# Performance work log

Measured on AMD Instinct MI355X. Metric: run time of the kernel, lower is better.

Reference implementation:

```python
import jax, jax.numpy as jnp
import numpy as np

N_PP = 100000   # papers
N_A = 50000     # authors
N_AP = N_PP + N_A
DIM = 16
B = 8192        # sampled node set sizes
E = 500000      # edges per modality
ALPHA = 0.5
EPS = 1e-12


def _cdist(x, y):
    # Euclidean cdist via quadratic expansion (avoids [N,M,d] intermediate)
    sq = (jnp.sum(x * x, -1)[:, None] + jnp.sum(y * y, -1)[None, :]
          - 2.0 * x @ y.T)
    return jnp.sqrt(jnp.maximum(sq, EPS))


def _pdist(x, y):
    d = x - y
    return jnp.sqrt(jnp.sum(d * d, -1) + EPS)


def setup_inputs() -> dict:
    key = jax.random.key(0)
    ks = jax.random.split(key, 10)
    u = lambda k, s: jax.random.uniform(k, s, jnp.float32, -1.0, 1.0)  # 2*rand-1
    p = u(ks[0], (N_PP, DIM))
    p_star = u(ks[1], (N_PP, DIM))
    a = u(ks[2], (N_A, DIM))
    beta_ap = u(ks[3], (N_AP,))
    gamma_pp = u(ks[4], (2 * N_PP,))
    edges_pp = jax.random.randint(ks[5], (2, E), 0, N_PP, jnp.int32)
    e_ap0 = jax.random.randint(ks[6], (1, E), 0, N_PP, jnp.int32)
    e_ap1 = jax.random.randint(ks[7], (1, E), N_PP, N_AP, jnp.int32)
    edges_ap = jnp.concatenate([e_ap0, e_ap1], 0)
    p_star_nodes = jnp.sort(jax.random.randint(ks[8], (B,), 0, N_PP, jnp.int32))
    kk = jax.random.split(ks[9], 2)
    p_nodes = jax.random.randint(kk[0], (B,), 0, N_PP, jnp.int32)
    a_nodes = jax.random.randint(kk[1], (B,), N_PP, N_AP, jnp.int32)
    return {"p": p, "p_star": p_star, "a": a, "beta_ap": beta_ap,
            "gamma_pp": gamma_pp, "edges_pp": edges_pp, "edges_ap": edges_ap,
            "p_star_nodes": p_star_nodes, "p_nodes": p_nodes, "a_nodes": a_nodes}


def reference(p, p_star, a, beta_ap, gamma_pp,
              edges_pp, edges_ap, p_star_nodes, p_nodes, a_nodes):
    # ---- pp modality ----
    # link term over edges (edges[0]=p_star idx, edges[1]=p idx)
    link_pp = jnp.sum(gamma_pp[edges_pp[0]] + gamma_pp[edges_pp[1] + N_PP]
                      - _pdist(p_star[edges_pp[0]], p[edges_pp[1]]))
    # non-link term: [B_pstar, B_p] matrix, upper-triangular (k=1) masked sum
    g_ps = gamma_pp[p_star_nodes]                 # [B]
    g_p = gamma_pp[p_nodes + N_PP]                # [B]
    mat_pp = g_ps[:, None] + g_p[None, :]         # == gamma_mat.T in torch code
    dist_pp = _cdist(p_star[p_star_nodes], p[p_nodes])
    nonlink_pp = jnp.sum(jnp.triu(jnp.exp(mat_pp - dist_pp), k=1))
    nll_pp = -(link_pp - nonlink_pp)

    # ---- ap modality ----
    link_ap = jnp.sum(beta_ap[edges_ap[0]] + beta_ap[edges_ap[1]]
                      - _pdist(p_star[edges_ap[0]], a[edges_ap[1] - N_PP]))
    b_ps = beta_ap[p_star_nodes]
    b_a = beta_ap[a_nodes]
    mat_ap = b_ps[:, None] + b_a[None, :]         # == beta_mat.T
    dist_ap = _cdist(p_star[p_star_nodes], a[a_nodes - N_PP])
    nonlink_ap = jnp.sum(jnp.exp(mat_ap - dist_ap))
    nll_ap = -(link_ap - nonlink_ap)

    # average batch loss as in __train_one_batch
    loss = ALPHA * nll_pp / B + (1.0 - ALPHA) * nll_ap / B
    return loss
```

## Files before the change

kernel.cpp:

```cpp
#include <hip/hip_runtime.h>

#define N_PP 100000
#define N_A  50000
#define NEDGE 500000
#define BSZ 8192
#define TILE 128
#define SCALE 1.44269504088896f
#define QS 127.0f
#define QSI (1.0f / 127.0f)

#define GRID_P 2048
#define EB 977
#define PP_JOBS 2080
#define AP_JOBS 4096
#define PJOBS (PP_JOBS + AP_JOBS)

#define GRID_FB 2048

typedef __attribute__((ext_vector_type(8)))  short bf16x8;
typedef __attribute__((ext_vector_type(16))) float f32x16;
typedef __attribute__((ext_vector_type(4)))  float f32x4;
typedef unsigned short u16;

#if __has_builtin(__builtin_amdgcn_sqrtf)
#define FAST_SQRT(x) __builtin_amdgcn_sqrtf(x)
#else
#define FAST_SQRT(x) sqrtf(x)
#endif
#if __has_builtin(__builtin_amdgcn_exp2f)
#define FAST_EXP2(x) __builtin_amdgcn_exp2f(x)
#else
#define FAST_EXP2(x) exp2f(x)
#endif

__device__ __forceinline__ u16 f2bf(float f) {
    unsigned u = __builtin_bit_cast(unsigned, f);
    u += 0x7FFFu + ((u >> 16) & 1u);
    return (u16)(u >> 16);
}
__device__ __forceinline__ float bf2f(u16 s) {
    unsigned u = ((unsigned)s) << 16;
    return __builtin_bit_cast(float, u);
}

__device__ __forceinline__ bf16x8 load_frag_f32(const float* __restrict__ src) {
    float4 v0 = *(const float4*)src;
    float4 v1 = *(const float4*)(src + 4);
    bf16x8 f;
    f[0] = (short)f2bf(v0.x); f[1] = (short)f2bf(v0.y);
    f[2] = (short)f2bf(v0.z); f[3] = (short)f2bf(v0.w);
    f[4] = (short)f2bf(v1.x); f[5] = (short)f2bf(v1.y);
    f[6] = (short)f2bf(v1.z); f[7] = (short)f2bf(v1.w);
    return f;
}

__device__ __forceinline__ int dot4i8(int a, int b, int c) {
#if __has_builtin(__builtin_amdgcn_sdot4)
    return __builtin_amdgcn_sdot4(a, b, c, false);
#else
    int s = c;
#pragma unroll
    for (int k = 0; k < 4; ++k) {
        int av = (int)(signed char)(a >> (8 * k));
        int bv = (int)(signed char)(b >> (8 * k));
        s += av * bv;
    }
    return s;
#endif
}

__device__ __forceinline__ float dist_i8(const int* __restrict__ ra,
                                         const int* __restrict__ rb) {
    int4 qa = *(const int4*)ra;
    int4 qb = *(const int4*)rb;
    int dot = dot4i8(qa.x, qb.x, 0);
    dot = dot4i8(qa.y, qb.y, dot);
    dot = dot4i8(qa.z, qb.z, dot);
    dot = dot4i8(qa.w, qb.w, dot);
    int na = dot4i8(qa.x, qa.x, 0);
    na = dot4i8(qa.y, qa.y, na);
    na = dot4i8(qa.z, qa.z, na);
    na = dot4i8(qa.w, qa.w, na);
    int nb = dot4i8(qb.x, qb.x, 0);
    nb = dot4i8(qb.y, qb.y, nb);
    nb = dot4i8(qb.z, qb.z, nb);
    nb = dot4i8(qb.w, qb.w, nb);
    int d2 = na + nb - 2 * dot;
    return FAST_SQRT((float)d2) * QSI;
}

__device__ __forceinline__ float pdist16_f32(const float* __restrict__ xv,
                                             const float* __restrict__ yv) {
    float d2 = 1e-12f;
#pragma unroll
    for (int c = 0; c < 16; c += 4) {
        float4 xq = *(const float4*)(xv + c);
        float4 yq = *(const float4*)(yv + c);
        float dx = xq.x - yq.x; d2 = fmaf(dx, dx, d2);
        float dy = xq.y - yq.y; d2 = fmaf(dy, dy, d2);
        float dz = xq.z - yq.z; d2 = fmaf(dz, dz, d2);
        float dw = xq.w - yq.w; d2 = fmaf(dw, dw, d2);
    }
    return sqrtf(d2);
}

__device__ __forceinline__ unsigned packq4(float a, float b, float c, float d) {
    int qa = (int)rintf(a * QS), qb = (int)rintf(b * QS);
    int qc = (int)rintf(c * QS), qd = (int)rintf(d * QS);
    return (unsigned)(qa & 0xFF) | ((unsigned)(qb & 0xFF) << 8)
         | ((unsigned)(qc & 0xFF) << 16) | ((unsigned)(qd & 0xFF) << 24);
}

__global__ __launch_bounds__(256) void prep_kernel(
        const float* __restrict__ p, const float* __restrict__ p_star,
        const float* __restrict__ a, const float* __restrict__ beta,
        const float* __restrict__ gamma,
        const int* __restrict__ psn, const int* __restrict__ pn,
        const int* __restrict__ an,
        int* __restrict__ ps8, int* __restrict__ p8, int* __restrict__ a8,
        u16* __restrict__ Xb, u16* __restrict__ Yp, u16* __restrict__ Ya,
        float* __restrict__ Xxx, float* __restrict__ Xg,
        float* __restrict__ Pyy, float* __restrict__ Pg,
        float* __restrict__ Ayy, float* __restrict__ Ag)
{
    const int NITEMS = 250000 + 3 * BSZ;
    for (int i = blockIdx.x * 256 + threadIdx.x; i < NITEMS; i += gridDim.x * 256) {
        if (i < 250000) {
            const float* src; int* dst;
            if (i < 100000)      { src = p_star + (size_t)i * 16;       dst = ps8 + (size_t)i * 4; }
            else if (i < 200000) { src = p + (size_t)(i - 100000) * 16; dst = p8 + (size_t)(i - 100000) * 4; }
            else                 { src = a + (size_t)(i - 200000) * 16; dst = a8 + (size_t)(i - 200000) * 4; }
            float4 v0 = *(const float4*)src;
            float4 v1 = *(const float4*)(src + 4);
            float4 v2 = *(const float4*)(src + 8);
            float4 v3 = *(const float4*)(src + 12);
            int4 q;
            q.x = (int)packq4(v0.x, v0.y, v0.z, v0.w);
            q.y = (int)packq4(v1.x, v1.y, v1.z, v1.w);
            q.z = (int)packq4(v2.x, v2.y, v2.z, v2.w);
            q.w = (int)packq4(v3.x, v3.y, v3.z, v3.w);
            *(int4*)dst = q;
        } else {
            const int j = i - 250000;
            const int which = j >> 13;
            const int r = j & (BSZ - 1);
            const float* src; float wsc; u16* drow; float* xxp; float* gp;
            if (which == 0) {
                int node = psn[r]; src = p_star + (size_t)node * 16;
                wsc = gamma[node] * SCALE; drow = Xb + (size_t)r * 16; xxp = Xxx; gp = Xg;
            } else if (which == 1) {
                int node = pn[r]; src = p + (size_t)node * 16;
                wsc = gamma[node + N_PP] * SCALE; drow = Yp + (size_t)r * 16; xxp = Pyy; gp = Pg;
            } else {
                int node = an[r]; src = a + (size_t)(node - N_PP) * 16;
                wsc = beta[node] * SCALE; drow = Ya + (size_t)r * 16; xxp = Ayy; gp = Ag;
            }
            bf16x8 lo = load_frag_f32(src);
            bf16x8 hi = load_frag_f32(src + 8);
            *(bf16x8*)drow = lo;
            *(bf16x8*)(drow + 8) = hi;
            float ss = 0.f;
#pragma unroll
            for (int c = 0; c < 8; ++c) {
                float q0 = bf2f((u16)lo[c]); ss = fmaf(q0, q0, ss);
                float q1 = bf2f((u16)hi[c]); ss = fmaf(q1, q1, ss);
            }
            xxp[r] = ss;
            gp[r] = wsc;
        }
    }
}

__global__ __launch_bounds__(256) void edge_kernel(
        const float* __restrict__ gamma, const float* __restrict__ beta,
        const int* __restrict__ edges_pp, const int* __restrict__ edges_ap,
        const int* __restrict__ ps8, const int* __restrict__ p8,
        const int* __restrict__ a8, float* __restrict__ epart)
{
    const int t = threadIdx.x;
    const int base = blockIdx.x * 512;
    float sppl = 0.f, sapl = 0.f;
#pragma unroll
    for (int k = 0; k < 2; ++k) {
        int i = base + k * 256 + t;
        if (i < NEDGE) {
            int e0 = __builtin_nontemporal_load(edges_pp + i);
            int e1 = __builtin_nontemporal_load(edges_pp + NEDGE + i);
            int f0 = __builtin_nontemporal_load(edges_ap + i);
            int f1 = __builtin_nontemporal_load(edges_ap + NEDGE + i);
            sppl += gamma[e0] + gamma[e1 + N_PP]
                  - dist_i8(ps8 + (size_t)e0 * 4, p8 + (size_t)e1 * 4);
            sapl += beta[f0] + beta[f1]
                  - dist_i8(ps8 + (size_t)f0 * 4, a8 + (size_t)(f1 - N_PP) * 4);
        }
    }
    __shared__ float red[4][2];
    const int l = t & 63, w = t >> 6;
#pragma unroll
    for (int o = 32; o > 0; o >>= 1) {
        sppl += __shfl_down(sppl, o, 64);
        sapl += __shfl_down(sapl, o, 64);
    }
    if (l == 0) { red[w][0] = sppl; red[w][1] = sapl; }
    __syncthreads();
    if (t < 2)
        epart[(size_t)blockIdx.x * 2 + t] =
            red[0][t] + red[1][t] + red[2][t] + red[3][t];
}

template <bool DIAG>
__device__ __forceinline__ float epi_rt(
        const f32x16& ca, const f32x16& cb,
        const float* __restrict__ xxg, const float* __restrict__ gxg,
        int rb, float yy0, float gy0, float yy1, float gy1,
        int cj0, int cj1)
{
    f32x4 xxq[4], gxq[4];
#pragma unroll
    for (int q = 0; q < 4; ++q) {
        xxq[q] = *(const f32x4*)&xxg[rb + q * 8];
        gxq[q] = *(const f32x4*)&gxg[rb + q * 8];
    }
    float s = 0.f;
#pragma unroll
    for (int q = 0; q < 4; ++q) {
#pragma unroll
        for (int j = 0; j < 4; ++j) {
            const int reg = q * 4 + j;
            float sxy = xxq[q][j];
            float gx  = gxq[q][j];
            float sq0 = fmaf(-2.f, ca[reg], sxy + yy0);
            float d0  = FAST_SQRT(fmaxf(sq0, 1e-12f));
            float v0  = FAST_EXP2(fmaf(-SCALE, d0, gx + gy0));
            float sq1 = fmaf(-2.f, cb[reg], sxy + yy1);
            float d1  = FAST_SQRT(fmaxf(sq1, 1e-12f));
            float v1  = FAST_EXP2(fmaf(-SCALE, d1, gx + gy1));
            if (DIAG) {
                int row = rb + q * 8 + j;
                v0 = (cj0 > row) ? v0 : 0.f;
                v1 = (cj1 > row) ? v1 : 0.f;
            }
            s += v0 + v1;
        }
    }
    return s;
}

__global__ __launch_bounds__(256) void pair_kernel(
        const u16* __restrict__ Xb, const u16* __restrict__ Yp,
        const u16* __restrict__ Ya,
        const float* __restrict__ Xxx, const float* __restrict__ Xg,
        const float* __restrict__ Pyy, const float* __restrict__ Pg,
        const float* __restrict__ Ayy, const float* __restrict__ Ag,
        float* __restrict__ ppart)
{
    const int t = threadIdx.x;
    const int l = t & 63, w = t >> 6;
    const int wr = w >> 1, wc = w & 1;
    const int l31 = l & 31, h = l >> 5;

    float s_ppn = 0.f, s_apn = 0.f;

    for (int j = blockIdx.x; j < PJOBS; j += gridDim.x) {
        const bool pp = (j < PP_JOBS);
        int bx, by;
        if (pp) {
            int k = j;
            float disc = sqrtf((float)(129 * 129 - 8 * k));
            by = (int)((129.0f - disc) * 0.5f);
            while (64 * by - (by * (by - 1)) / 2 > k) --by;
            while (64 * (by + 1) - ((by + 1) * by) / 2 <= k) ++by;
            bx = by + (k - (64 * by - (by * (by - 1)) / 2));
        } else {
            int k = j - PP_JOBS;
            bx = k & 63; by = k >> 6;
        }
        const bool diag = pp && (bx == by);

        const u16* Ytab = pp ? Yp : Ya;
        const float* yyP = (pp ? Pyy : Ayy) + bx * TILE;
        const float* gyP = (pp ? Pg  : Ag ) + bx * TILE;
        const int ar0 = by * TILE + wr * 64 + l31;
        const int bc0 = bx * TILE + wc * 64 + l31;
        bf16x8 aF0 = *(const bf16x8*)(Xb   + (size_t)ar0 * 16 + h * 8);
        bf16x8 aF1 = *(const bf16x8*)(Xb   + (size_t)(ar0 + 32) * 16 + h * 8);
        bf16x8 bF0 = *(const bf16x8*)(Ytab + (size_t)bc0 * 16 + h * 8);
        bf16x8 bF1 = *(const bf16x8*)(Ytab + (size_t)(bc0 + 32) * 16 + h * 8);
        const float* xxg = Xxx + by * TILE;
        const float* gxg = Xg  + by * TILE;
        const int cj0 = wc * 64 + l31, cj1 = cj0 + 32;
        const float yy0 = yyP[cj0], gy0 = gyP[cj0];
        const float yy1 = yyP[cj1], gy1 = gyP[cj1];
        const int rb0 = wr * 64 + 4 * h, rb1 = rb0 + 32;

        f32x16 c00, c01, c10, c11;
#pragma unroll
        for (int i = 0; i < 16; ++i) { c00[i] = 0.f; c01[i] = 0.f; c10[i] = 0.f; c11[i] = 0.f; }
        c00 = __builtin_amdgcn_mfma_f32_32x32x16_bf16(aF0, bF0, c00, 0, 0, 0);
        c01 = __builtin_amdgcn_mfma_f32_32x32x16_bf16(aF0, bF1, c01, 0, 0, 0);
        c10 = __builtin_amdgcn_mfma_f32_32x32x16_bf16(aF1, bF0, c10, 0, 0, 0);
        c11 = __builtin_amdgcn_mfma_f32_32x32x16_bf16(aF1, bF1, c11, 0, 0, 0);

        float sum;
        if (diag) {
            sum = epi_rt<true >(c00, c01, xxg, gxg, rb0, yy0, gy0, yy1, gy1, cj0, cj1)
                + epi_rt<true >(c10, c11, xxg, gxg, rb1, yy0, gy0, yy1, gy1, cj0, cj1);
        } else {
            sum = epi_rt<false>(c00, c01, xxg, gxg, rb0, yy0, gy0, yy1, gy1, cj0, cj1)
                + epi_rt<false>(c10, c11, xxg, gxg, rb1, yy0, gy0, yy1, gy1, cj0, cj1);
        }
        if (pp) s_ppn += sum; else s_apn += sum;
    }

    __shared__ float red[4][2];
#pragma unroll
    for (int o = 32; o > 0; o >>= 1) {
        s_ppn += __shfl_down(s_ppn, o, 64);
        s_apn += __shfl_down(s_apn, o, 64);
    }
    if (l == 0) { red[w][0] = s_ppn; red[w][1] = s_apn; }
    __syncthreads();
    if (t < 2)
        ppart[(size_t)blockIdx.x * 2 + t] =
            red[0][t] + red[1][t] + red[2][t] + red[3][t];
}

__global__ __launch_bounds__(256) void finalize_split(
        const float* __restrict__ epart, const float* __restrict__ ppart,
        float* __restrict__ out)
{
    __shared__ double acc4[4];
    const int t = threadIdx.x;
    const int c = t >> 6, l = t & 63;
    double s = 0.0;
    if (c == 0)      { for (int i = l; i < EB; i += 64)     s += (double)epart[(size_t)i * 2 + 0]; }
    else if (c == 1) { for (int i = l; i < GRID_P; i += 64) s += (double)ppart[(size_t)i * 2 + 0]; }
    else if (c == 2) { for (int i = l; i < EB; i += 64)     s += (double)epart[(size_t)i * 2 + 1]; }
    else             { for (int i = l; i < GRID_P; i += 64) s += (double)ppart[(size_t)i * 2 + 1]; }
#pragma unroll
    for (int o = 32; o > 0; o >>= 1) s += __shfl_down(s, o, 64);
    if (l == 0) acc4[c] = s;
    __syncthreads();
    if (t == 0) {
        double nll_pp = -(acc4[0] - acc4[1]);
        double nll_ap = -(acc4[2] - acc4[3]);
        out[0] = (float)(0.5 * nll_pp / (double)BSZ + 0.5 * nll_ap / (double)BSZ);
    }
}

__global__ __launch_bounds__(256) void fused_fb(
        const float* __restrict__ p, const float* __restrict__ p_star,
        const float* __restrict__ a, const float* __restrict__ beta,
        const float* __restrict__ gamma,
        const int* __restrict__ edges_pp, const int* __restrict__ edges_ap,
        const int* __restrict__ psn, const int* __restrict__ pn,
        const int* __restrict__ an, float* __restrict__ partials)
{
    const int t = threadIdx.x;
    const int l = t & 63, w = t >> 6;
    const int wr = w >> 1, wc = w & 1;
    const int l31 = l & 31, h = l >> 5;

    __shared__ float sxx[TILE], sgx[TILE], syy[TILE], sgy[TILE];
    __shared__ float red4[4][4];

    float s_ppl = 0.f, s_ppn = 0.f, s_apl = 0.f, s_apn = 0.f;
    const int NJ = EB + PP_JOBS + AP_JOBS;

    for (int j = blockIdx.x; j < NJ; j += gridDim.x) {
        if (j < EB) {
            const int base = j * 512;
#pragma unroll
            for (int k = 0; k < 2; ++k) {
                int i = base + k * 256 + t;
                if (i < NEDGE) {
                    int e0 = edges_pp[i], e1 = edges_pp[NEDGE + i];
                    int f0 = edges_ap[i], f1 = edges_ap[NEDGE + i];
                    s_ppl += gamma[e0] + gamma[e1 + N_PP]
                           - pdist16_f32(p_star + (size_t)e0 * 16, p + (size_t)e1 * 16);
                    s_apl += beta[f0] + beta[f1]
                           - pdist16_f32(p_star + (size_t)f0 * 16, a + (size_t)(f1 - N_PP) * 16);
                }
            }
        } else {
            const bool pp = (j < EB + PP_JOBS);
            int bx, by;
            if (pp) {
                int k = j - EB;
                float disc = sqrtf((float)(129 * 129 - 8 * k));
                by = (int)((129.0f - disc) * 0.5f);
                while (64 * by - (by * (by - 1)) / 2 > k) --by;
                while (64 * (by + 1) - ((by + 1) * by) / 2 <= k) ++by;
                bx = by + (k - (64 * by - (by * (by - 1)) / 2));
            } else {
                int k = j - EB - PP_JOBS;
                bx = k & 63; by = k >> 6;
            }
            const bool diag = pp && (bx == by);
            const float* Y  = pp ? p : a;
            const float* wv = pp ? gamma : beta;
            const int* yn   = pp ? pn : an;
            const int wyo   = pp ? N_PP : 0;
            const int yvo   = pp ? 0 : -N_PP;
            const int ar0 = by * TILE + wr * 64 + l31;
            const int an0 = psn[ar0], an1 = psn[ar0 + 32];
            bf16x8 aF0 = load_frag_f32(p_star + (size_t)an0 * 16 + h * 8);
            bf16x8 aF1 = load_frag_f32(p_star + (size_t)an1 * 16 + h * 8);
            const int bc0g = bx * TILE + wc * 64 + l31;
            const int bn0 = yn[bc0g], bn1 = yn[bc0g + 32];
            bf16x8 bF0 = load_frag_f32(Y + (size_t)(bn0 + yvo) * 16 + h * 8);
            bf16x8 bF1 = load_frag_f32(Y + (size_t)(bn1 + yvo) * 16 + h * 8);
            {
                const bool isx = (t < 128);
                const int  r   = isx ? t : t - 128;
                const int  node = isx ? psn[by * TILE + r] : yn[bx * TILE + r];
                const float* src = isx ? (p_star + (size_t)node * 16)
                                       : (Y + (size_t)(node + yvo) * 16);
                float ss = 0.f;
#pragma unroll
                for (int c = 0; c < 16; c += 4) {
                    float4 v = *(const float4*)(src + c);
                    float q0 = bf2f(f2bf(v.x)), q1 = bf2f(f2bf(v.y));
                    float q2 = bf2f(f2bf(v.z)), q3 = bf2f(f2bf(v.w));
                    ss = fmaf(q0, q0, ss); ss = fmaf(q1, q1, ss);
                    ss = fmaf(q2, q2, ss); ss = fmaf(q3, q3, ss);
                }
                if (isx) { sxx[r] = ss; sgx[r] = wv[node] * SCALE; }
                else     { syy[r] = ss; sgy[r] = wv[node + wyo] * SCALE; }
            }
            __syncthreads();
            const int cj0 = wc * 64 + l31, cj1 = cj0 + 32;
            const float yy0 = syy[cj0], gy0 = sgy[cj0];
            const float yy1 = syy[cj1], gy1 = sgy[cj1];
            const int rb0 = wr * 64 + 4 * h, rb1 = rb0 + 32;

            f32x16 c00, c01, c10, c11;
#pragma unroll
            for (int i = 0; i < 16; ++i) { c00[i] = 0.f; c01[i] = 0.f; c10[i] = 0.f; c11[i] = 0.f; }
            c00 = __builtin_amdgcn_mfma_f32_32x32x16_bf16(aF0, bF0, c00, 0, 0, 0);
            c01 = __builtin_amdgcn_mfma_f32_32x32x16_bf16(aF0, bF1, c01, 0, 0, 0);
            c10 = __builtin_amdgcn_mfma_f32_32x32x16_bf16(aF1, bF0, c10, 0, 0, 0);
            c11 = __builtin_amdgcn_mfma_f32_32x32x16_bf16(aF1, bF1, c11, 0, 0, 0);

            float sum;
            if (diag) {
                sum = epi_rt<true >(c00, c01, sxx, sgx, rb0, yy0, gy0, yy1, gy1, cj0, cj1)
                    + epi_rt<true >(c10, c11, sxx, sgx, rb1, yy0, gy0, yy1, gy1, cj0, cj1);
            } else {
                sum = epi_rt<false>(c00, c01, sxx, sgx, rb0, yy0, gy0, yy1, gy1, cj0, cj1)
                    + epi_rt<false>(c10, c11, sxx, sgx, rb1, yy0, gy0, yy1, gy1, cj0, cj1);
            }
            if (pp) s_ppn += sum; else s_apn += sum;
            __syncthreads();
        }
    }

    float v4[4] = {s_ppl, s_ppn, s_apl, s_apn};
#pragma unroll
    for (int c = 0; c < 4; ++c) {
        float r = v4[c];
#pragma unroll
        for (int o = 32; o > 0; o >>= 1) r += __shfl_down(r, o, 64);
        if (l == 0) red4[w][c] = r;
    }
    __syncthreads();
    if (t < 4)
        partials[(size_t)blockIdx.x * 4 + t] =
            red4[0][t] + red4[1][t] + red4[2][t] + red4[3][t];
}

__global__ __launch_bounds__(256) void finalize_fb(
        const float* __restrict__ partials, float* __restrict__ out)
{
    __shared__ double acc4[4];
    const int t = threadIdx.x;
    const int c = t >> 6, l = t & 63;
    double s = 0.0;
    for (int i = l; i < GRID_FB; i += 64) s += (double)partials[(size_t)i * 4 + c];
#pragma unroll
    for (int o = 32; o > 0; o >>= 1) s += __shfl_down(s, o, 64);
    if (l == 0) acc4[c] = s;
    __syncthreads();
    if (t == 0) {
        double nll_pp = -(acc4[0] - acc4[1]);
        double nll_ap = -(acc4[2] - acc4[3]);
        out[0] = (float)(0.5 * nll_pp / (double)BSZ + 0.5 * nll_ap / (double)BSZ);
    }
}

extern "C" void kernel_launch(void* const* d_in, const int* in_sizes, int n_in,
                              void* d_out, int out_size, void* d_ws, size_t ws_size,
                              hipStream_t stream)
{
    const float* p       = (const float*)d_in[0];
    const float* p_star  = (const float*)d_in[1];
    const float* a       = (const float*)d_in[2];
    const float* beta    = (const float*)d_in[3];
    const float* gamma   = (const float*)d_in[4];
    const int* edges_pp  = (const int*)d_in[5];
    const int* edges_ap  = (const int*)d_in[6];
    const int* psn       = (const int*)d_in[7];
    const int* pn        = (const int*)d_in[8];
    const int* an        = (const int*)d_in[9];

    char* ws = (char*)d_ws;
    size_t off = 0;
    float* ppart = (float*)(ws + off); off += (size_t)GRID_P * 2 * sizeof(float);
    float* epart = (float*)(ws + off); off += (size_t)EB * 2 * sizeof(float);
    int* ps8 = (int*)(ws + off); off += (size_t)100000 * 16;
    int* p8  = (int*)(ws + off); off += (size_t)100000 * 16;
    int* a8  = (int*)(ws + off); off += (size_t)50000 * 16;
    u16* Xb  = (u16*)(ws + off); off += (size_t)BSZ * 32;
    u16* Yp  = (u16*)(ws + off); off += (size_t)BSZ * 32;
    u16* Ya  = (u16*)(ws + off); off += (size_t)BSZ * 32;
    float* Xxx = (float*)(ws + off); off += BSZ * 4;
    float* Xg  = (float*)(ws + off); off += BSZ * 4;
    float* Pyy = (float*)(ws + off); off += BSZ * 4;
    float* Pg  = (float*)(ws + off); off += BSZ * 4;
    float* Ayy = (float*)(ws + off); off += BSZ * 4;
    float* Ag  = (float*)(ws + off); off += BSZ * 4;
    const bool packed = (ws_size >= off);

    if (packed) {
        prep_kernel<<<256, 256, 0, stream>>>(
            p, p_star, a, beta, gamma, psn, pn, an,
            ps8, p8, a8, Xb, Yp, Ya, Xxx, Xg, Pyy, Pg, Ayy, Ag);
        edge_kernel<<<EB, 256, 0, stream>>>(
            gamma, beta, edges_pp, edges_ap, ps8, p8, a8, epart);
        pair_kernel<<<GRID_P, 256, 0, stream>>>(
            Xb, Yp, Ya, Xxx, Xg, Pyy, Pg, Ayy, Ag, ppart);
        finalize_split<<<1, 256, 0, stream>>>(epart, ppart, (float*)d_out);
    } else {
        float* fbpart = (float*)ws;
        fused_fb<<<GRID_FB, 256, 0, stream>>>(
            p, p_star, a, beta, gamma, edges_pp, edges_ap, psn, pn, an, fbpart);
        finalize_fb<<<1, 256, 0, stream>>>(fbpart, (float*)d_out);
    }
}
```

Baseline: 86.25 us.

## Merge edge and pair kernels into one interleaved work kernel

Fuses the edge-sum kernel and the MFMA pair kernel into a single launch. Every third block among the first 3*EB handles an edge chunk and the rest run pair jobs, so memory-bound gather work shares the GPU with compute-bound tiles. This is meant to remove one launch and the idle tail between the two kernels. The prep kernel grid is also doubled. Register and LDS usage become the maximum of both paths, which could lower occupancy.

```diff
diff --git a/kernel.cpp b/kernel.cpp
--- a/kernel.cpp
+++ b/kernel.cpp
@@ -9,8 +9,9 @@
 #define QS 127.0f
 #define QSI (1.0f / 127.0f)
 
+#define EB 977
 #define GRID_P 2048
-#define EB 977
+#define GRID_W (3 * EB + GRID_P - EB)
 #define PP_JOBS 2080
 #define AP_JOBS 4096
 #define PJOBS (PP_JOBS + AP_JOBS)
@@ -171,43 +172,6 @@
     }
 }
 
-__global__ __launch_bounds__(256) void edge_kernel(
-        const float* __restrict__ gamma, const float* __restrict__ beta,
-        const int* __restrict__ edges_pp, const int* __restrict__ edges_ap,
-        const int* __restrict__ ps8, const int* __restrict__ p8,
-        const int* __restrict__ a8, float* __restrict__ epart)
-{
-    const int t = threadIdx.x;
-    const int base = blockIdx.x * 512;
-    float sppl = 0.f, sapl = 0.f;
-#pragma unroll
-    for (int k = 0; k < 2; ++k) {
-        int i = base + k * 256 + t;
-        if (i < NEDGE) {
-            int e0 = __builtin_nontemporal_load(edges_pp + i);
-            int e1 = __builtin_nontemporal_load(edges_pp + NEDGE + i);
-            int f0 = __builtin_nontemporal_load(edges_ap + i);
-            int f1 = __builtin_nontemporal_load(edges_ap + NEDGE + i);
-            sppl += gamma[e0] + gamma[e1 + N_PP]
-                  - dist_i8(ps8 + (size_t)e0 * 4, p8 + (size_t)e1 * 4);
-            sapl += beta[f0] + beta[f1]
-                  - dist_i8(ps8 + (size_t)f0 * 4, a8 + (size_t)(f1 - N_PP) * 4);
-        }
-    }
-    __shared__ float red[4][2];
-    const int l = t & 63, w = t >> 6;
-#pragma unroll
-    for (int o = 32; o > 0; o >>= 1) {
-        sppl += __shfl_down(sppl, o, 64);
-        sapl += __shfl_down(sapl, o, 64);
-    }
-    if (l == 0) { red[w][0] = sppl; red[w][1] = sapl; }
-    __syncthreads();
-    if (t < 2)
-        epart[(size_t)blockIdx.x * 2 + t] =
-            red[0][t] + red[1][t] + red[2][t] + red[3][t];
-}
-
 template <bool DIAG>
 __device__ __forceinline__ float epi_rt(
         const f32x16& ca, const f32x16& cb,
@@ -246,22 +210,61 @@
     return s;
 }
 
-__global__ __launch_bounds__(256) void pair_kernel(
+__global__ __launch_bounds__(256) void work_kernel(
+        const float* __restrict__ gamma, const float* __restrict__ beta,
+        const int* __restrict__ edges_pp, const int* __restrict__ edges_ap,
+        const int* __restrict__ ps8, const int* __restrict__ p8,
+        const int* __restrict__ a8,
         const u16* __restrict__ Xb, const u16* __restrict__ Yp,
         const u16* __restrict__ Ya,
         const float* __restrict__ Xxx, const float* __restrict__ Xg,
         const float* __restrict__ Pyy, const float* __restrict__ Pg,
         const float* __restrict__ Ayy, const float* __restrict__ Ag,
-        float* __restrict__ ppart)
-{
+        float* __restrict__ epart, float* __restrict__ ppart)
+{
+    const int b = blockIdx.x;
     const int t = threadIdx.x;
     const int l = t & 63, w = t >> 6;
+
+    if ((b % 3 == 0) && (b / 3 < EB)) {
+        const int base = (b / 3) * 512;
+        float sppl = 0.f, sapl = 0.f;
+#pragma unroll
+        for (int k = 0; k < 2; ++k) {
+            int i = base + k * 256 + t;
+            if (i < NEDGE) {
+                int e0 = __builtin_nontemporal_load(edges_pp + i);
+                int e1 = __builtin_nontemporal_load(edges_pp + NEDGE + i);
+                int f0 = __builtin_nontemporal_load(edges_ap + i);
+                int f1 = __builtin_nontemporal_load(edges_ap + NEDGE + i);
+                sppl += gamma[e0] + gamma[e1 + N_PP]
+                      - dist_i8(ps8 + (size_t)e0 * 4, p8 + (size_t)e1 * 4);
+                sapl += beta[f0] + beta[f1]
+                      - dist_i8(ps8 + (size_t)f0 * 4, a8 + (size_t)(f1 - N_PP) * 4);
+            }
+        }
+        __shared__ float rede[4][2];
+#pragma unroll
+        for (int o = 32; o > 0; o >>= 1) {
+            sppl += __shfl_down(sppl, o, 64);
+            sapl += __shfl_down(sapl, o, 64);
+        }
+        if (l == 0) { rede[w][0] = sppl; rede[w][1] = sapl; }
+        __syncthreads();
+        if (t < 2)
+            epart[(size_t)(b / 3) * 2 + t] =
+                rede[0][t] + rede[1][t] + rede[2][t] + rede[3][t];
+        return;
+    }
+
+    const int pid = (b < 3 * EB) ? (b - b / 3 - 1) : (b - EB);
+
     const int wr = w >> 1, wc = w & 1;
     const int l31 = l & 31, h = l >> 5;
 
     float s_ppn = 0.f, s_apn = 0.f;
 
-    for (int j = blockIdx.x; j < PJOBS; j += gridDim.x) {
+    for (int j = pid; j < PJOBS; j += GRID_P) {
         const bool pp = (j < PP_JOBS);
         int bx, by;
         if (pp) {
@@ -312,17 +315,17 @@
         if (pp) s_ppn += sum; else s_apn += sum;
     }
 
-    __shared__ float red[4][2];
+    __shared__ float redp[4][2];
 #pragma unroll
     for (int o = 32; o > 0; o >>= 1) {
         s_ppn += __shfl_down(s_ppn, o, 64);
         s_apn += __shfl_down(s_apn, o, 64);
     }
-    if (l == 0) { red[w][0] = s_ppn; red[w][1] = s_apn; }
+    if (l == 0) { redp[w][0] = s_ppn; redp[w][1] = s_apn; }
     __syncthreads();
     if (t < 2)
-        ppart[(size_t)blockIdx.x * 2 + t] =
-            red[0][t] + red[1][t] + red[2][t] + red[3][t];
+        ppart[(size_t)pid * 2 + t] =
+            redp[0][t] + redp[1][t] + redp[2][t] + redp[3][t];
 }
 
 __global__ __launch_bounds__(256) void finalize_split(
@@ -522,13 +525,12 @@
     const bool packed = (ws_size >= off);
 
     if (packed) {
-        prep_kernel<<<256, 256, 0, stream>>>(
+        prep_kernel<<<512, 256, 0, stream>>>(
             p, p_star, a, beta, gamma, psn, pn, an,
             ps8, p8, a8, Xb, Yp, Ya, Xxx, Xg, Pyy, Pg, Ayy, Ag);
-        edge_kernel<<<EB, 256, 0, stream>>>(
-            gamma, beta, edges_pp, edges_ap, ps8, p8, a8, epart);
-        pair_kernel<<<GRID_P, 256, 0, stream>>>(
-            Xb, Yp, Ya, Xxx, Xg, Pyy, Pg, Ayy, Ag, ppart);
+        work_kernel<<<EB + GRID_P, 256, 0, stream>>>(
+            gamma, beta, edges_pp, edges_ap, ps8, p8, a8,
+            Xb, Yp, Ya, Xxx, Xg, Pyy, Pg, Ayy, Ag, epart, ppart);
         finalize_split<<<1, 256, 0, stream>>>(epart, ppart, (float*)d_out);
     } else {
         float* fbpart = (float*)ws;
```

After: 82.43 us. -4.4%, faster.
